# Performance work log

Measured on AMD Instinct MI355X. Metric: run time of the kernel, lower is better.

## Reference

```python
import jax, jax.numpy as jnp
import numpy as np

B, T, D = 4, 2048, 1024  # batch, seq_len, dec_dim_in == dim_proj_QK == dim_proj_V == dec_dim_out


def setup_inputs() -> dict:
    key = jax.random.key(0)
    ks = jax.random.split(key, 9)
    s = 1.0 / np.sqrt(D)  # torch Linear default init scale
    return {
        "x": jax.random.normal(ks[0], (B, T, D), dtype=jnp.float32),
        "Wq": jax.random.uniform(ks[1], (D, D), jnp.float32, -s, s),
        "bq": jax.random.uniform(ks[2], (D,), jnp.float32, -s, s),
        "Wk": jax.random.uniform(ks[3], (D, D), jnp.float32, -s, s),
        "bk": jax.random.uniform(ks[4], (D,), jnp.float32, -s, s),
        "Wv": jax.random.uniform(ks[5], (D, D), jnp.float32, -s, s),
        "bv": jax.random.uniform(ks[6], (D,), jnp.float32, -s, s),
        "Wh": jax.random.uniform(ks[7], (D, D), jnp.float32, -s, s),
        "bh": jax.random.uniform(ks[8], (D,), jnp.float32, -s, s),
    }


def reference(x, Wq, bq, Wk, bk, Wv, bv, Wh, bh):
    Q = x @ Wq + bq                      # [B, T, Dqk]
    K = x @ Wk + bk                      # [B, T, Dqk]
    V = x @ Wv + bv                      # [B, T, Dv]
    scale = 1.0 / jnp.sqrt(jnp.asarray(K.shape[-1], x.dtype))
    scores = jnp.einsum("btd,bsd->bts", Q, K) * scale  # [B, T, T]
    t = K.shape[1]
    causal = jnp.triu(jnp.ones((t, t), dtype=bool), k=1)  # True above diagonal
    scores = jnp.where(causal[None, :, :], -jnp.inf, scores)
    attn = jax.nn.softmax(scores, axis=-1)
    # dropout is identity in eval mode (reference baseline)
    out = jnp.einsum("bts,bsd->btd", attn, V)  # [B, T, Dv]
    return out @ Wh + bh
```

## Files before the change

kernel.cpp:

```cpp
#include <hip/hip_runtime.h>


typedef __attribute__((ext_vector_type(8)))  short short8;
typedef __attribute__((ext_vector_type(4)))  float f4;
typedef __attribute__((ext_vector_type(8)))  unsigned short us8;

#define BM 128
#define BN 128
#define BK 64

#define F_OBF    1
#define F_SKIP   2
#define F_KLIM   4
#define F_REVY   8
#define F_VSPL   16
#define F_RSCL   32
#define F_EXP    64
#define F_RSUM   128
#define F_SPLITK 256

__device__ inline unsigned short f2bf(float f) {
    union { float f; unsigned u; } c; c.f = f;
    unsigned u = c.u;
    return (unsigned short)((u + 0x7fffu + ((u >> 16) & 1u)) >> 16);
}
__device__ inline float bf2f(unsigned short u) {
    union { unsigned u; float f; } c; c.u = ((unsigned)u) << 16;
    return c.f;
}
__device__ inline void gload16(const void* g, void* l) {
    __builtin_amdgcn_global_load_lds(
        (const __attribute__((address_space(1))) void*)g,
        (__attribute__((address_space(3))) void*)l,
        16, 0, 0);
}

template<int FLAGS>
__global__ __launch_bounds__(256)
void gemm_bt(const unsigned short* __restrict__ A,
             const unsigned short* __restrict__ Bt,
             void* __restrict__ C,
             const float* __restrict__ bias,
             int M, int N, int K, int lda, int ldb, int ldc,
             long sA, long sB, long sC,
             float scale,
             unsigned short* __restrict__ C2, long sC2, int Tv, int vsplit,
             float* __restrict__ rowsums)
{
    const int b = blockIdx.z;
    A  += (long)b * sA;
    Bt += (long)b * sB;
    if (FLAGS & (F_RSCL | F_RSUM)) rowsums += (long)b * M;

    int by = blockIdx.y;
    if (FLAGS & F_REVY) by = gridDim.y - 1 - by;
    const int m0 = by * BM;

    int n0, split = 0;
    if (FLAGS & F_SPLITK) {
        const int nbx = N / BN;
        n0 = (blockIdx.x % nbx) * BN;
        split = blockIdx.x / nbx;
        if (split && m0 < 1024) return;
    } else {
        n0 = blockIdx.x * BN;
    }

    if ((FLAGS & F_SKIP) && n0 > m0 + (BM - 1)) return;

    int kend = K;
    if (FLAGS & F_KLIM) { int ke = m0 + BM; kend = ke < K ? ke : K; }
    int kt0 = 0;
    if (FLAGS & F_SPLITK) {
        if (split == 0) { if (kend > 1024) kend = 1024; }
        else            { kt0 = 1024 / BK; }
    }
    const int kt1 = kend / BK;

    __shared__ unsigned short As[BM * BK];
    __shared__ unsigned short Bs[BN * BK];

    const int tid  = threadIdx.x;
    const int lane = tid & 63;
    const int wave = tid >> 6;
    const int wm   = wave & 1;
    const int wn   = wave >> 1;
    const int lrow = lane & 15;
    const int quad = lane >> 4;

    f4 acc[4][4];
#pragma unroll
    for (int i = 0; i < 4; ++i)
#pragma unroll
        for (int j = 0; j < 4; ++j) acc[i][j] = (f4)0.0f;

    const int srow = tid >> 3;
    const int gco  = ((tid & 7) ^ (srow & 7)) << 3;
    const int rdsl = (lrow & 7);

    for (int kt = kt0; kt < kt1; ++kt) {
        const int k0 = kt * BK;
#pragma unroll
        for (int d = 0; d < 4; ++d) {
            const int row = d * 32 + srow;
            const unsigned short* ga = A  + (long)(m0 + row) * lda + k0 + gco;
            const unsigned short* gb = Bt + (long)(n0 + row) * ldb + k0 + gco;
            const int ldsoff = (d * 256 + wave * 64) * 16;
            gload16(ga, (char*)As + ldsoff);
            gload16(gb, (char*)Bs + ldsoff);
        }
        __syncthreads();

#pragma unroll
        for (int ks = 0; ks < 2; ++ks) {
            const int slot = ((ks * 4 + quad) ^ rdsl) << 3;
            short8 af[4], bfr[4];
#pragma unroll
            for (int i = 0; i < 4; ++i) {
                af[i]  = *(const short8*)(As + (wm * 64 + i * 16 + lrow) * BK + slot);
                bfr[i] = *(const short8*)(Bs + (wn * 64 + i * 16 + lrow) * BK + slot);
            }
#pragma unroll
            for (int i = 0; i < 4; ++i)
#pragma unroll
                for (int j = 0; j < 4; ++j)
                    acc[i][j] = __builtin_amdgcn_mfma_f32_16x16x32_bf16(
                        af[i], bfr[j], acc[i][j], 0, 0, 0);
        }
        __syncthreads();
    }

    const int row0 = m0 + wm * 64 + quad * 4;
    const int col0 = n0 + wn * 64 + lrow;

    float bj[4];
#pragma unroll
    for (int j = 0; j < 4; ++j) bj[j] = bias ? bias[col0 + j * 16] : 0.0f;

    if ((FLAGS & F_VSPL) && n0 >= vsplit) {
        const int bidx  = m0 >> 11;
        const int tloc0 = (m0 & 2047) + wm * 64 + quad * 4;
#pragma unroll
        for (int j = 0; j < 4; ++j) {
            const int d = col0 + j * 16 - vsplit;
            unsigned short* base = C2 + (long)bidx * sC2 + (long)d * Tv;
#pragma unroll
            for (int i = 0; i < 4; ++i) {
                const int tt = tloc0 + i * 16;
                unsigned long long pk = 0;
#pragma unroll
                for (int r = 0; r < 4; ++r) {
                    float v = acc[i][j][r] * scale + bj[j];
                    pk |= (unsigned long long)f2bf(v) << (16 * r);
                }
                *(unsigned long long*)(base + tt) = pk;
            }
        }
        return;
    }

    float inv[16];
    if (FLAGS & F_RSCL) {
#pragma unroll
        for (int i = 0; i < 4; ++i)
#pragma unroll
            for (int r = 0; r < 4; ++r)
                inv[i * 4 + r] = 1.0f / rowsums[row0 + i * 16 + r];
    }

    float rs[16];
    if (FLAGS & F_RSUM) {
#pragma unroll
        for (int k = 0; k < 16; ++k) rs[k] = 0.0f;
    }

    unsigned short* Cb = (unsigned short*)C;
    float*          Cf = ((FLAGS & F_SPLITK) && split) ? (float*)C2 : (float*)C;
    const long cbase = (long)b * sC;

#pragma unroll
    for (int i = 0; i < 4; ++i) {
#pragma unroll
        for (int j = 0; j < 4; ++j) {
            const int col = col0 + j * 16;
#pragma unroll
            for (int r = 0; r < 4; ++r) {
                const int row = row0 + i * 16 + r;
                float v = acc[i][j][r] * scale;
                if (FLAGS & F_EXP) { v = __expf(v); if (col > row) v = 0.0f; }
                if (FLAGS & F_RSUM) rs[i * 4 + r] += v;
                if (FLAGS & F_RSCL) v *= inv[i * 4 + r];
                if (!((FLAGS & F_SPLITK) && split)) v += bj[j];
                const long off = cbase + (long)row * ldc + col;
                if (FLAGS & F_OBF) Cb[off] = f2bf(v);
                else               Cf[off] = v;
            }
        }
    }

    if (FLAGS & F_RSUM) {
#pragma unroll
        for (int k = 0; k < 16; ++k) {
            rs[k] += __shfl_xor(rs[k], 1);
            rs[k] += __shfl_xor(rs[k], 2);
            rs[k] += __shfl_xor(rs[k], 4);
            rs[k] += __shfl_xor(rs[k], 8);
        }
        if (lrow == 0) {
#pragma unroll
            for (int i = 0; i < 4; ++i)
#pragma unroll
                for (int r = 0; r < 4; ++r)
                    atomicAdd(&rowsums[row0 + i * 16 + r], rs[i * 4 + r]);
        }
    }
}

__global__ void combine_upper(float* __restrict__ out,
                              const float* __restrict__ part)
{
    const long base = ((long)blockIdx.y * 2048 + 1024) * 1024 / 4;
    const long i = base + blockIdx.x * 256 + threadIdx.x;
    f4 a = ((f4*)out)[i];
    f4 bb = ((const f4*)part)[i];
    a.x += bb.x; a.y += bb.y; a.z += bb.z; a.w += bb.w;
    ((f4*)out)[i] = a;
}

__global__ void gemv_bhh(const unsigned short* __restrict__ Wht,
                         const float* __restrict__ bv,
                         const float* __restrict__ bh,
                         float* __restrict__ bhh)
{
    const int m = blockIdx.x;
    const int tid = threadIdx.x;
    const int lane = tid & 63, wave = tid >> 6;
    __shared__ float red[4];
    const unsigned short* row = Wht + (long)m * 1024;
    float s = 0.0f;
#pragma unroll
    for (int k = 0; k < 4; ++k) {
        const int idx = tid * 4 + k;
        s += bf2f(row[idx]) * bv[idx];
    }
    for (int o = 32; o > 0; o >>= 1) s += __shfl_down(s, o);
    if (lane == 0) red[wave] = s;
    __syncthreads();
    if (tid == 0) bhh[m] = red[0] + red[1] + red[2] + red[3] + bh[m];
}

__global__ void prep(const float* __restrict__ x,
                     const float* __restrict__ Wq, const float* __restrict__ Wk,
                     const float* __restrict__ Wv, const float* __restrict__ Wh,
                     const float* __restrict__ bq, const float* __restrict__ bk,
                     unsigned short* __restrict__ Xbf,
                     unsigned short* __restrict__ Wqkvt,
                     unsigned short* __restrict__ Wht,
                     unsigned short* __restrict__ Wvb,
                     float* __restrict__ bqkv)
{
    __shared__ unsigned short tsh[32][33];
    const int bid = blockIdx.x;
    const int tid = threadIdx.x;

    if (bid < 8192) {
        const int i = bid * 256 + tid;
        f4 v = ((const f4*)x)[i];
        unsigned long long p = (unsigned long long)f2bf(v.x)
                             | ((unsigned long long)f2bf(v.y) << 16)
                             | ((unsigned long long)f2bf(v.z) << 32)
                             | ((unsigned long long)f2bf(v.w) << 48);
        ((unsigned long long*)Xbf)[i] = p;
    } else if (bid < 9216) {
        const int i = (bid - 8192) * 256 + tid;
        f4 v = ((const f4*)Wv)[i];
        unsigned long long p = (unsigned long long)f2bf(v.x)
                             | ((unsigned long long)f2bf(v.y) << 16)
                             | ((unsigned long long)f2bf(v.z) << 32)
                             | ((unsigned long long)f2bf(v.w) << 48);
        ((unsigned long long*)Wvb)[i] = p;
    } else if (bid < 12288) {
        const int wi = bid - 9216;
        const int w = wi >> 10, tile = wi & 1023;
        const float* src = (w == 0) ? Wq : (w == 1) ? Wk : Wh;
        unsigned short* dst = (w == 0) ? Wqkvt : (w == 1) ? (Wqkvt + 1024 * 1024) : Wht;
        const int c0 = (tile & 31) * 32, r0 = (tile >> 5) * 32;
        const int xx = tid & 31, yy = tid >> 5;
        for (int i = yy; i < 32; i += 8)
            tsh[i][xx] = f2bf(src[(long)(r0 + i) * 1024 + c0 + xx]);
        __syncthreads();
        for (int i = yy; i < 32; i += 8)
            dst[(long)(c0 + i) * 1024 + r0 + xx] = tsh[xx][i];
    } else {
        const int i = (bid - 12288) * 256 + tid;
        if (i < 1024) { bqkv[i] = bq[i]; bqkv[1024 + i] = bk[i]; bqkv[2048 + i] = 0.0f; }
    }
}

extern "C" void kernel_launch(void* const* d_in, const int* in_sizes, int n_in,
                              void* d_out, int out_size, void* d_ws, size_t ws_size,
                              hipStream_t stream)
{
    const float* x  = (const float*)d_in[0];
    const float* Wq = (const float*)d_in[1];
    const float* bq = (const float*)d_in[2];
    const float* Wk = (const float*)d_in[3];
    const float* bk = (const float*)d_in[4];
    const float* Wv = (const float*)d_in[5];
    const float* bv = (const float*)d_in[6];
    const float* Wh = (const float*)d_in[7];
    const float* bh = (const float*)d_in[8];
    float* out = (float*)d_out;

    const int  Bb = 4, T = 2048, Dm = 1024;
    const long BT = (long)Bb * T;

    unsigned short* ws = (unsigned short*)d_ws;
    size_t o = 0;
    unsigned short* Xbf   = ws + o; o += (size_t)BT * Dm;
    unsigned short* Wqkvt = ws + o; o += (size_t)3 * Dm * Dm;
    unsigned short* Wht   = ws + o; o += (size_t)Dm * Dm;
    unsigned short* Wvb   = ws + o; o += (size_t)Dm * Dm;
    float* bqkv = (float*)(ws + o); o += (size_t)3 * Dm * 2;
    float* bhh  = (float*)(ws + o); o += (size_t)Dm * 2;
    float* sums = (float*)(ws + o); o += (size_t)BT * 2;
    unsigned short* QKV   = ws + o; o += (size_t)BT * 3 * Dm;
    unsigned short* Vt    = ws + o; o += (size_t)BT * Dm;
    unsigned short* Pp    = ws + o; o += (size_t)Bb * T * T;
    float* part = (float*)(ws + o);

    const dim3 blk(256);
    const long sRow3 = (long)T * 3 * Dm;

    hipMemsetAsync(sums, 0, (size_t)BT * sizeof(float), stream);

    prep<<<12289, blk, 0, stream>>>(x, Wq, Wk, Wv, Wh, bq, bk,
                                    Xbf, Wqkvt, Wht, Wvb, bqkv);

    gemm_bt<F_OBF><<<dim3(Dm / BN, Dm / BM, 1), blk, 0, stream>>>(
        Wht, Wvb, Wqkvt + 2 * Dm * Dm, nullptr, Dm, Dm, Dm, Dm, Dm, Dm,
        0, 0, 0, 1.0f, nullptr, 0, 0, 0, nullptr);

    gemv_bhh<<<Dm, blk, 0, stream>>>(Wht, bv, bh, bhh);

    gemm_bt<F_OBF | F_VSPL><<<dim3(3 * Dm / BN, BT / BM, 1), blk, 0, stream>>>(
        Xbf, Wqkvt, QKV, bqkv, (int)BT, 3 * Dm, Dm, Dm, Dm, 3 * Dm,
        0, 0, 0, 1.0f, Vt, (long)Dm * T, T, 2 * Dm, nullptr);

    gemm_bt<F_OBF | F_SKIP | F_REVY | F_EXP | F_RSUM>
        <<<dim3(T / BN, T / BM, Bb), blk, 0, stream>>>(
        QKV, QKV + Dm, Pp, nullptr, T, T, Dm, 3 * Dm, 3 * Dm, T,
        sRow3, sRow3, (long)T * T, 1.0f / 32.0f,
        nullptr, 0, 0, 0, sums);

    gemm_bt<F_KLIM | F_REVY | F_RSCL | F_SPLITK>
        <<<dim3(2 * Dm / BN, T / BM, Bb), blk, 0, stream>>>(
        Pp, Vt, out, bhh, T, Dm, T, T, T, Dm,
        (long)T * T, (long)Dm * T, (long)T * Dm, 1.0f,
        (unsigned short*)part, 0, 0, 0, sums);

    combine_upper<<<dim3(1024, Bb), blk, 0, stream>>>(out, part);
}
```

Baseline: 308.6 us.

## Add 256x256 tiled 8-wave GEMM with double-buffered LDS and MFMA priority scheduling

Introduces a new gemm256 kernel with 256x256 tiles, 512 threads and two-stage direct-to-LDS prefetch using explicit vmcnt waits and barriers. MFMA phases are interleaved with LDS fragment loads under raised s_setprio. The QKV projection, the causal score/exp, and the PV GEMM now use it. The old gemm_bt is stripped down to a plain bias epilogue that only the Wh*Wv fold still uses. Row-sum reciprocals move into a separate small kernel so the PV epilogue only multiplies. Larger tiles raise data reuse per block but coarsen the causal skipping, halve the number of blocks, and increase register pressure.

```diff
diff --git a/kernel.cpp b/kernel.cpp
--- a/kernel.cpp
+++ b/kernel.cpp
@@ -3,11 +3,12 @@
 
 typedef __attribute__((ext_vector_type(8)))  short short8;
 typedef __attribute__((ext_vector_type(4)))  float f4;
-typedef __attribute__((ext_vector_type(8)))  unsigned short us8;
 
 #define BM 128
 #define BN 128
 #define BK 64
+#define BM2 256
+#define BN2 256
 
 #define F_OBF    1
 #define F_SKIP   2
@@ -18,6 +19,10 @@
 #define F_EXP    64
 #define F_RSUM   128
 #define F_SPLITK 256
+
+#define WAITV8() asm volatile("s_waitcnt vmcnt(8)" ::: "memory")
+#define WAITV0() asm volatile("s_waitcnt vmcnt(0)" ::: "memory")
+#define BARR()   asm volatile("s_barrier" ::: "memory")
 
 __device__ inline unsigned short f2bf(float f) {
     union { float f; unsigned u; } c; c.f = f;
@@ -137,15 +142,213 @@
 #pragma unroll
     for (int j = 0; j < 4; ++j) bj[j] = bias ? bias[col0 + j * 16] : 0.0f;
 
+    unsigned short* Cb = (unsigned short*)C;
+    float*          Cf = (float*)C;
+    const long cbase = (long)b * sC;
+
+#pragma unroll
+    for (int i = 0; i < 4; ++i) {
+#pragma unroll
+        for (int j = 0; j < 4; ++j) {
+            const int col = col0 + j * 16;
+#pragma unroll
+            for (int r = 0; r < 4; ++r) {
+                const int row = row0 + i * 16 + r;
+                float v = acc[i][j][r] * scale + bj[j];
+                const long off = cbase + (long)row * ldc + col;
+                if (FLAGS & F_OBF) Cb[off] = f2bf(v);
+                else               Cf[off] = v;
+            }
+        }
+    }
+}
+
+template<int HA>
+__device__ inline void lda_half(short8 (&af)[8], const unsigned short* Asb,
+                                int wm, int lrow, int quad, int rdsl)
+{
+#pragma unroll
+    for (int i = 0; i < 4; ++i)
+#pragma unroll
+        for (int ks = 0; ks < 2; ++ks)
+            af[i * 2 + ks] = *(const short8*)(
+                Asb + (wm * 128 + HA * 64 + i * 16 + lrow) * BK
+                    + (((ks * 4 + quad) ^ rdsl) << 3));
+}
+
+template<int QB>
+__device__ inline void ldb_q(short8 (&bq)[4], const unsigned short* Bsb,
+                             int wn, int lrow, int quad, int rdsl)
+{
+#pragma unroll
+    for (int j = 0; j < 2; ++j)
+#pragma unroll
+        for (int ks = 0; ks < 2; ++ks)
+            bq[j * 2 + ks] = *(const short8*)(
+                Bsb + (wn * 64 + QB * 32 + j * 16 + lrow) * BK
+                    + (((ks * 4 + quad) ^ rdsl) << 3));
+}
+
+template<int HA, int QB>
+__device__ inline void mfma16(f4 (&acc)[8][4], const short8 (&af)[8],
+                              const short8 (&bq)[4])
+{
+#pragma unroll
+    for (int i = 0; i < 4; ++i)
+#pragma unroll
+        for (int j = 0; j < 2; ++j)
+#pragma unroll
+            for (int ks = 0; ks < 2; ++ks)
+                acc[HA * 4 + i][QB * 2 + j] =
+                    __builtin_amdgcn_mfma_f32_16x16x32_bf16(
+                        af[i * 2 + ks], bq[j * 2 + ks],
+                        acc[HA * 4 + i][QB * 2 + j], 0, 0, 0);
+}
+
+__device__ inline void stage_tile256(const unsigned short* __restrict__ Arow,
+                                     const unsigned short* __restrict__ Brow,
+                                     int k0, unsigned short* As, unsigned short* Bs,
+                                     int lda, int ldb, int tid)
+{
+    const int srow = tid >> 3;
+    const int gco  = ((tid & 7) ^ (srow & 7)) << 3;
+    const int wave = tid >> 6;
+#pragma unroll
+    for (int d = 0; d < 4; ++d) {
+        const int row = d * 64 + srow;
+        const int ldsoff = (d * 512 + wave * 64) * 16;
+        gload16(Arow + (long)row * lda + k0 + gco, (char*)As + ldsoff);
+        gload16(Brow + (long)row * ldb + k0 + gco, (char*)Bs + ldsoff);
+    }
+}
+
+template<int FLAGS>
+__global__ __launch_bounds__(512)
+void gemm256(const unsigned short* __restrict__ A,
+             const unsigned short* __restrict__ Bt,
+             void* __restrict__ C,
+             const float* __restrict__ bias,
+             int M, int N, int K, int lda, int ldb, int ldc,
+             long sA, long sB, long sC,
+             float scale,
+             unsigned short* __restrict__ C2, long sC2, int Tv, int vsplit,
+             float* __restrict__ rowsums)
+{
+    const int b = blockIdx.z;
+    A  += (long)b * sA;
+    Bt += (long)b * sB;
+    if (FLAGS & (F_RSCL | F_RSUM)) rowsums += (long)b * M;
+
+    int by = blockIdx.y;
+    if (FLAGS & F_REVY) by = gridDim.y - 1 - by;
+    const int m0 = by * BM2;
+
+    int n0, split = 0;
+    if (FLAGS & F_SPLITK) {
+        const int nbx = N / BN2;
+        n0 = (blockIdx.x % nbx) * BN2;
+        split = blockIdx.x / nbx;
+        if (split && m0 < 1024) return;
+    } else {
+        n0 = blockIdx.x * BN2;
+    }
+
+    if ((FLAGS & F_SKIP) && n0 > m0 + (BM2 - 1)) return;
+
+    int kend = K;
+    if (FLAGS & F_KLIM) { int ke = m0 + BM2; kend = ke < K ? ke : K; }
+    int kt0 = 0;
+    if (FLAGS & F_SPLITK) {
+        if (split == 0) { if (kend > 1024) kend = 1024; }
+        else            { kt0 = 1024 / BK; }
+    }
+    const int kt1 = kend / BK;
+
+    __shared__ unsigned short sm[4][BM2 * BK];
+
+    const int tid  = threadIdx.x;
+    const int lane = tid & 63;
+    const int wave = tid >> 6;
+    const int wm   = wave & 1;
+    const int wn   = wave >> 1;
+    const int lrow = lane & 15;
+    const int quad = lane >> 4;
+    const int rdsl = lrow & 7;
+
+    f4 acc[8][4];
+#pragma unroll
+    for (int i = 0; i < 8; ++i)
+#pragma unroll
+        for (int j = 0; j < 4; ++j) acc[i][j] = (f4)0.0f;
+
+    const unsigned short* Arow = A  + (long)m0 * lda;
+    const unsigned short* Brow = Bt + (long)n0 * ldb;
+    const int ktiles = kt1 - kt0;
+
+    stage_tile256(Arow, Brow, kt0 * BK, sm[0], sm[1], lda, ldb, tid);
+    if (ktiles > 1) {
+        stage_tile256(Arow, Brow, (kt0 + 1) * BK, sm[2], sm[3], lda, ldb, tid);
+        WAITV8();
+    } else {
+        WAITV0();
+    }
+    BARR();
+
+    short8 af[8], bf0[4], bf1[4];
+    for (int t = 0; t < ktiles; ++t) {
+        const int cur = t & 1;
+        const unsigned short* Asb = sm[cur * 2];
+        const unsigned short* Bsb = sm[cur * 2 + 1];
+
+        lda_half<0>(af, Asb, wm, lrow, quad, rdsl);
+        ldb_q<0>(bf0, Bsb, wn, lrow, quad, rdsl);
+        BARR();
+        __builtin_amdgcn_s_setprio(1);
+        mfma16<0, 0>(acc, af, bf0);
+        __builtin_amdgcn_s_setprio(0);
+        BARR();
+
+        ldb_q<1>(bf1, Bsb, wn, lrow, quad, rdsl);
+        BARR();
+        __builtin_amdgcn_s_setprio(1);
+        mfma16<0, 1>(acc, af, bf1);
+        __builtin_amdgcn_s_setprio(0);
+        BARR();
+
+        lda_half<1>(af, Asb, wm, lrow, quad, rdsl);
+        BARR();
+        __builtin_amdgcn_s_setprio(1);
+        mfma16<1, 1>(acc, af, bf1);
+        __builtin_amdgcn_s_setprio(0);
+        BARR();
+
+        if (t + 2 < ktiles)
+            stage_tile256(Arow, Brow, (kt0 + t + 2) * BK,
+                          sm[cur * 2], sm[cur * 2 + 1], lda, ldb, tid);
+        __builtin_amdgcn_s_setprio(1);
+        mfma16<1, 0>(acc, af, bf0);
+        __builtin_amdgcn_s_setprio(0);
+        if (t + 2 < ktiles) WAITV8();
+        else                WAITV0();
+        BARR();
+    }
+
+    const int row0 = m0 + wm * 128 + quad * 4;
+    const int col0 = n0 + wn * 64 + lrow;
+
+    float bj[4];
+#pragma unroll
+    for (int j = 0; j < 4; ++j) bj[j] = bias ? bias[col0 + j * 16] : 0.0f;
+
     if ((FLAGS & F_VSPL) && n0 >= vsplit) {
         const int bidx  = m0 >> 11;
-        const int tloc0 = (m0 & 2047) + wm * 64 + quad * 4;
+        const int tloc0 = (m0 & 2047) + wm * 128 + quad * 4;
 #pragma unroll
         for (int j = 0; j < 4; ++j) {
             const int d = col0 + j * 16 - vsplit;
             unsigned short* base = C2 + (long)bidx * sC2 + (long)d * Tv;
 #pragma unroll
-            for (int i = 0; i < 4; ++i) {
+            for (int i = 0; i < 8; ++i) {
                 const int tt = tloc0 + i * 16;
                 unsigned long long pk = 0;
 #pragma unroll
@@ -159,19 +362,19 @@
         return;
     }
 
-    float inv[16];
+    float inv[32];
     if (FLAGS & F_RSCL) {
 #pragma unroll
-        for (int i = 0; i < 4; ++i)
+        for (int i = 0; i < 8; ++i)
 #pragma unroll
             for (int r = 0; r < 4; ++r)
-                inv[i * 4 + r] = 1.0f / rowsums[row0 + i * 16 + r];
-    }
-
-    float rs[16];
+                inv[i * 4 + r] = rowsums[row0 + i * 16 + r];
+    }
+
+    float rs[32];
     if (FLAGS & F_RSUM) {
 #pragma unroll
-        for (int k = 0; k < 16; ++k) rs[k] = 0.0f;
+        for (int k = 0; k < 32; ++k) rs[k] = 0.0f;
     }
 
     unsigned short* Cb = (unsigned short*)C;
@@ -179,7 +382,7 @@
     const long cbase = (long)b * sC;
 
 #pragma unroll
-    for (int i = 0; i < 4; ++i) {
+    for (int i = 0; i < 8; ++i) {
 #pragma unroll
         for (int j = 0; j < 4; ++j) {
             const int col = col0 + j * 16;
@@ -200,7 +403,7 @@
 
     if (FLAGS & F_RSUM) {
 #pragma unroll
-        for (int k = 0; k < 16; ++k) {
+        for (int k = 0; k < 32; ++k) {
             rs[k] += __shfl_xor(rs[k], 1);
             rs[k] += __shfl_xor(rs[k], 2);
             rs[k] += __shfl_xor(rs[k], 4);
@@ -208,7 +411,7 @@
         }
         if (lrow == 0) {
 #pragma unroll
-            for (int i = 0; i < 4; ++i)
+            for (int i = 0; i < 8; ++i)
 #pragma unroll
                 for (int r = 0; r < 4; ++r)
                     atomicAdd(&rowsums[row0 + i * 16 + r], rs[i * 4 + r]);
@@ -225,6 +428,12 @@
     f4 bb = ((const f4*)part)[i];
     a.x += bb.x; a.y += bb.y; a.z += bb.z; a.w += bb.w;
     ((f4*)out)[i] = a;
+}
+
+__global__ void recip_sums(float* __restrict__ s)
+{
+    const int i = blockIdx.x * 256 + threadIdx.x;
+    s[i] = 1.0f / s[i];
 }
 
 __global__ void gemv_bhh(const unsigned short* __restrict__ Wht,
@@ -330,6 +539,7 @@
     float* part = (float*)(ws + o);
 
     const dim3 blk(256);
+    const dim3 blk2(512);
     const long sRow3 = (long)T * 3 * Dm;
 
     hipMemsetAsync(sums, 0, (size_t)BT * sizeof(float), stream);
@@ -343,18 +553,20 @@
 
     gemv_bhh<<<Dm, blk, 0, stream>>>(Wht, bv, bh, bhh);
 
-    gemm_bt<F_OBF | F_VSPL><<<dim3(3 * Dm / BN, BT / BM, 1), blk, 0, stream>>>(
+    gemm256<F_OBF | F_VSPL><<<dim3(3 * Dm / BN2, BT / BM2, 1), blk2, 0, stream>>>(
         Xbf, Wqkvt, QKV, bqkv, (int)BT, 3 * Dm, Dm, Dm, Dm, 3 * Dm,
         0, 0, 0, 1.0f, Vt, (long)Dm * T, T, 2 * Dm, nullptr);
 
-    gemm_bt<F_OBF | F_SKIP | F_REVY | F_EXP | F_RSUM>
-        <<<dim3(T / BN, T / BM, Bb), blk, 0, stream>>>(
+    gemm256<F_OBF | F_SKIP | F_REVY | F_EXP | F_RSUM>
+        <<<dim3(T / BN2, T / BM2, Bb), blk2, 0, stream>>>(
         QKV, QKV + Dm, Pp, nullptr, T, T, Dm, 3 * Dm, 3 * Dm, T,
         sRow3, sRow3, (long)T * T, 1.0f / 32.0f,
         nullptr, 0, 0, 0, sums);
 
-    gemm_bt<F_KLIM | F_REVY | F_RSCL | F_SPLITK>
-        <<<dim3(2 * Dm / BN, T / BM, Bb), blk, 0, stream>>>(
+    recip_sums<<<dim3((int)(BT / 256)), blk, 0, stream>>>(sums);
+
+    gemm256<F_KLIM | F_REVY | F_RSCL | F_SPLITK>
+        <<<dim3(2 * Dm / BN2, T / BM2, Bb), blk2, 0, stream>>>(
         Pp, Vt, out, bhh, T, Dm, T, T, T, Dm,
         (long)T * T, (long)Dm * T, (long)T * Dm, 1.0f,
         (unsigned short*)part, 0, 0, 0, sums);
```

New measurement: 299.5 us. 1.03x faster.
